# Kernel optimization log

Measured on AMD Instinct MI355X. Metric: run time of the kernel, lower is better.

The kernel has to match this reference:

```python
import jax, jax.numpy as jnp
import numpy as np

NTOKEN, NINP, NHID = 50257, 256, 256
B, T = 64, 2048
RES, FC1 = 10, NHID // 3
EPS = 1e-5

def lrelu(x, p=0.01):
    return jnp.maximum(x, x * p)

def setup_inputs() -> dict:
    key = jax.random.key(0)
    ks = jax.random.split(key, 12)
    s = 0.05
    inp = {
        "input": jax.random.randint(ks[0], (B, T), 0, NTOKEN),
        "hx": jnp.zeros((B, NHID), jnp.float32),
        "cx": jnp.zeros((B, NHID), jnp.float32),
        "seq_len": jax.random.randint(ks[1], (B,), 1, T + 1),  # lengths in [1, T]
        "emb_w": jax.random.uniform(ks[2], (NTOKEN, NINP), jnp.float32, -0.1, 0.1),
        "W_ih": jax.random.normal(ks[3], (4 * NHID, NINP), jnp.float32) * s,
        "W_hh": jax.random.normal(ks[4], (4 * NHID, NHID), jnp.float32) * s,
        "b_ih": jnp.zeros((4 * NHID,), jnp.float32),
        "b_hh": jnp.zeros((4 * NHID,), jnp.float32),
        "rfc1_w": jax.random.normal(ks[5], (RES, NHID), jnp.float32) * s,
        "rfc1_b": jnp.zeros((RES,), jnp.float32),
        "rbn_g": jnp.ones((RES,), jnp.float32),
        "rbn_b": jnp.zeros((RES,), jnp.float32),
        "rbn_rm": jnp.zeros((RES,), jnp.float32),
        "rbn_rv": jnp.ones((RES,), jnp.float32),
        "rfc2_w": jax.random.normal(ks[6], (NHID, RES), jnp.float32) * s,
        "rfc2_b": jnp.zeros((NHID,), jnp.float32),
        "fc1_w": jax.random.normal(ks[7], (FC1, NHID), jnp.float32) * s,
        "fc1_b": jnp.zeros((FC1,), jnp.float32),
        "bn1_g": jnp.ones((FC1,), jnp.float32),
        "bn1_b": jnp.zeros((FC1,), jnp.float32),
        "bn1_rm": jnp.zeros((FC1,), jnp.float32),
        "bn1_rv": jnp.ones((FC1,), jnp.float32),
        "fc2_w": jax.random.normal(ks[8], (2, FC1), jnp.float32) * s,
        "fc2_b": jnp.zeros((2,), jnp.float32),
    }
    return inp

def reference(input, hx, cx, seq_len, emb_w, W_ih, W_hh, b_ih, b_hh,
              rfc1_w, rfc1_b, rbn_g, rbn_b, rbn_rm, rbn_rv, rfc2_w, rfc2_b,
              fc1_w, fc1_b, bn1_g, bn1_b, bn1_rm, bn1_rv, fc2_w, fc2_b):
    # eval mode: dropout = identity, noise = 0, BatchNorm uses running stats
    emb = emb_w[input.T]  # [T, B, ninp]
    # precompute input-side gates once (batched matmul) -> [T, B, 4*nhid]
    x_gates = jnp.einsum('tbi,gi->tbg', emb, W_ih) + b_ih + b_hh

    def step(carry, xg):
        h, c = carry
        gates = xg + h @ W_hh.T
        i, f, g, o = jnp.split(gates, 4, axis=-1)
        c = jax.nn.sigmoid(f) * c + jax.nn.sigmoid(i) * jnp.tanh(g)
        h = jax.nn.sigmoid(o) * jnp.tanh(c)
        return (h, c), h

    (hx_f, cx_f), outs = jax.lax.scan(step, (hx, cx), x_gates)  # outs: [T, B, nhid]

    # ragged mean pooling over first seq_len[b] steps
    mask = (jnp.arange(T)[:, None] < seq_len[None, :]).astype(outs.dtype)  # [T, B]
    feature = jnp.einsum('tbh,tb->bh', outs, mask) / seq_len[:, None].astype(outs.dtype)

    # ResNet block (eval)
    res = jax.nn.relu(feature) @ rfc1_w.T + rfc1_b
    res = jax.nn.relu(res)
    res = (res - rbn_rm) * jax.lax.rsqrt(rbn_rv + EPS) * rbn_g + rbn_b
    feature = feature + res @ rfc2_w.T + rfc2_b

    # classifier head
    fc = feature @ fc1_w.T + fc1_b
    fc = (fc - bn1_rm) * jax.lax.rsqrt(bn1_rv + EPS) * bn1_g + bn1_b
    fc = lrelu(fc)
    logits = fc @ fc2_w.T + fc2_b
    logp = jax.nn.log_softmax(logits, axis=-1)
    return (logp, hx_f, cx_f)
```

## Files before the change

### kernel.cpp

```cpp
#include <hip/hip_runtime.h>
#include <cstdint>


#define NTOKEN 50257
#define NINP 256
#define NHID 256
#define BB 64
#define TT 2048
#define NRES 10
#define NFC1 85
#define EPSV 1e-5f

typedef _Float16 f16;
typedef _Float16 f16x2 __attribute__((ext_vector_type(2)));
typedef _Float16 f16x8 __attribute__((ext_vector_type(8)));
typedef float f32x4 __attribute__((ext_vector_type(4)));

static __device__ __forceinline__ float sigm(float x) { return 1.0f / (1.0f + __expf(-x)); }
static __device__ __forceinline__ float tanh_(float x) {
  float ax = fabsf(x);
  float e = __expf(-2.0f * ax);
  float t = (1.0f - e) / (1.0f + e);
  return x < 0.0f ? -t : t;
}

static __device__ __forceinline__ float fdot2(f16x2 a, f16x2 b, float c) {
#if __has_builtin(__builtin_amdgcn_fdot2)
  return __builtin_amdgcn_fdot2(a, b, c, false);
#else
  return c + (float)a[0] * (float)b[0] + (float)a[1] * (float)b[1];
#endif
}

__global__ void k0_convert(const float* __restrict__ emb_w, const float* __restrict__ W_ih,
                           const float* __restrict__ b_ih, const float* __restrict__ b_hh,
                           f16* __restrict__ emb16, f16* __restrict__ wih16,
                           float* __restrict__ bias) {
  int64_t i = (int64_t)blockIdx.x * blockDim.x + threadIdx.x;
  if (i < (int64_t)NTOKEN * NINP) emb16[i] = (f16)emb_w[i];
  if (i < 4 * NHID * NINP) wih16[i] = (f16)W_ih[i];
  if (i < 4 * NHID) bias[i] = b_ih[i] + b_hh[i];
}

__global__ __launch_bounds__(256) void k1_gemm(const f16* __restrict__ emb16,
                                               const f16* __restrict__ wih16,
                                               const float* __restrict__ bias,
                                               f16* __restrict__ xgtab) {
  __shared__ __align__(16) f16 a_lds[64][40];
  __shared__ __align__(16) f16 b_lds[256][40];
  const int mt = blockIdx.x;
  const int nt0 = blockIdx.y * 256;
  const int tid = threadIdx.x;
  const int lane = tid & 63;
  const int w = tid >> 6;
  const int quad = lane >> 4;
  const int l16 = lane & 15;

  f32x4 acc[16];
#pragma unroll
  for (int i = 0; i < 16; i++) acc[i] = (f32x4){0.f, 0.f, 0.f, 0.f};

  const int ar = tid >> 2;
  int av = mt * 64 + ar;
  if (av > NTOKEN - 1) av = NTOKEN - 1;
  const int ac = (tid & 3) * 8;

  for (int kb = 0; kb < 256; kb += 32) {
    *(uint4*)&a_lds[ar][ac] = *(const uint4*)&emb16[av * 256 + kb + ac];
    {
      const uint4* bs = (const uint4*)&wih16[(nt0 + tid) * 256 + kb];
      uint4* bd = (uint4*)&b_lds[tid][0];
      bd[0] = bs[0]; bd[1] = bs[1]; bd[2] = bs[2]; bd[3] = bs[3];
    }
    __syncthreads();
    f16x8 af = *(const f16x8*)&a_lds[w * 16 + l16][quad * 8];
#pragma unroll
    for (int nt = 0; nt < 16; nt++) {
      f16x8 bf = *(const f16x8*)&b_lds[nt * 16 + l16][quad * 8];
      acc[nt] = __builtin_amdgcn_mfma_f32_16x16x32_f16(af, bf, acc[nt], 0, 0, 0);
    }
    __syncthreads();
  }
#pragma unroll
  for (int nt = 0; nt < 16; nt++) {
#pragma unroll
    for (int rg = 0; rg < 4; rg++) {
      int v = mt * 64 + w * 16 + quad * 4 + rg;
      if (v < NTOKEN) {
        int n = nt0 + nt * 16 + l16;
        xgtab[v * 1024 + n] = (f16)(acc[nt][rg] + bias[n]);
      }
    }
  }
}

#define RK 100
#define LKW ((128 - RK) / 2)
__global__ __attribute__((amdgpu_flat_work_group_size(512, 512), amdgpu_waves_per_eu(2, 2)))
void k2_rnn(
    const int* __restrict__ input, const float* __restrict__ hx0,
    const float* __restrict__ cx0, const int* __restrict__ seq_len,
    const float* __restrict__ Whh, const f16* __restrict__ xgtab,
    float* __restrict__ feat, float* __restrict__ out_hx, float* __restrict__ out_cx) {
  __shared__ uint4 lw4[LKW * 512];
  __shared__ __align__(16) f16 hpak[2][NHID];

  const int b = blockIdx.x;
  const int tid = threadIdx.x;
  const int w = tid >> 6;
  const int lane = tid & 63;
  const int half = lane >> 5;
  const int p = w * 32 + (lane & 31);
  const int r0 = half ? (p + 256) : p;
  const int r1 = half ? (p + 768) : (p + 512);

  unsigned int w0[RK], w1[RK];
  unsigned int pa0 = 0, pd0 = 0;
#pragma unroll
  for (int m = 0; m < 128; m++) {
    float2 a = *(const float2*)&Whh[r0 * 256 + 2 * m];
    float2 d = *(const float2*)&Whh[r1 * 256 + 2 * m];
    f16x2 pa; pa[0] = (f16)a.x; pa[1] = (f16)a.y;
    f16x2 pd; pd[0] = (f16)d.x; pd[1] = (f16)d.y;
    unsigned int ua = __builtin_bit_cast(unsigned int, pa);
    unsigned int ud = __builtin_bit_cast(unsigned int, pd);
    if (m < RK) {
      w0[m] = ua; w1[m] = ud;
    } else if (((m - RK) & 1) == 0) {
      pa0 = ua; pd0 = ud;
    } else {
      lw4[((m - RK) >> 1) * 512 + tid] = make_uint4(pa0, pd0, ua, ud);
    }
  }

  float c = 0.0f, pool = 0.0f, hnew = 0.0f;
  if (tid < NHID) hpak[0][tid] = (f16)hx0[b * NHID + tid];
  if (!half) c = cx0[b * NHID + p];
  const int L = seq_len[b];
  __syncthreads();

  const int* tokp = input + b * TT;
  int tok_next = tokp[1];
  f16 xga, xgb;
  {
    int tok0 = tokp[0];
    xga = xgtab[tok0 * 1024 + r0];
    xgb = xgtab[tok0 * 1024 + r1];
  }

  for (int t = 0; t < TT; t++) {
    const int cur = t & 1;
    int tn = (t + 2 < TT) ? tokp[t + 2] : 0;
    f16 pfa = xgtab[tok_next * 1024 + r0];
    f16 pfb = xgtab[tok_next * 1024 + r1];

    float acc0 = (float)xga, acc1 = (float)xgb;
    const uint4* hp = (const uint4*)hpak[cur];
    uint4 hC = hp[0];
    uint4 hN = hp[1];
#pragma unroll
    for (int mb = 0; mb < 32; mb++) {
      uint4 h4 = hC;
      hC = hN;
      if (mb < 30) hN = hp[mb + 2];
      uint4 ww0, ww1;
      if (4 * mb >= RK) {
        ww0 = lw4[(2 * (mb - RK / 4)) * 512 + tid];
        ww1 = lw4[(2 * (mb - RK / 4) + 1) * 512 + tid];
      }
#pragma unroll
      for (int j = 0; j < 4; j++) {
        const int m = mb * 4 + j;
        unsigned int hu = (j == 0) ? h4.x : (j == 1) ? h4.y : (j == 2) ? h4.z : h4.w;
        f16x2 hh = __builtin_bit_cast(f16x2, hu);
        f16x2 wa, wb;
        if (m < RK) {
          wa = __builtin_bit_cast(f16x2, w0[m]);
          wb = __builtin_bit_cast(f16x2, w1[m]);
        } else {
          unsigned int uwa = (j == 0) ? ww0.x : (j == 1) ? ww0.z : (j == 2) ? ww1.x : ww1.z;
          unsigned int uwb = (j == 0) ? ww0.y : (j == 1) ? ww0.w : (j == 2) ? ww1.y : ww1.w;
          wa = __builtin_bit_cast(f16x2, uwa);
          wb = __builtin_bit_cast(f16x2, uwb);
        }
        acc0 = fdot2(wa, hh, acc0);
        acc1 = fdot2(wb, hh, acc1);
      }
    }

    float s0 = sigm(acc0);
    float oa = 0.0f;
    if (half) oa = sigm(acc1);
    float fs = __shfl_xor(half ? s0 : 0.0f, 32);
    float os = __shfl_xor(oa, 32);
    if (!half) {
      float gg = tanh_(acc1);
      c = fs * c + s0 * gg;
      hnew = os * tanh_(c);
      if (t < L) pool += hnew;
      hpak[cur ^ 1][p] = (f16)hnew;
    }
    __syncthreads();
    xga = pfa; xgb = pfb; tok_next = tn;
  }

  if (!half) {
    feat[b * NHID + p] = pool / (float)L;
    out_hx[b * NHID + p] = hnew;
    out_cx[b * NHID + p] = c;
  }
}

__global__ __launch_bounds__(256) void k3_head(const float* __restrict__ feat,
    const float* __restrict__ rfc1_w, const float* __restrict__ rfc1_b,
    const float* __restrict__ rbn_g, const float* __restrict__ rbn_b,
    const float* __restrict__ rbn_rm, const float* __restrict__ rbn_rv,
    const float* __restrict__ rfc2_w, const float* __restrict__ rfc2_b,
    const float* __restrict__ fc1_w, const float* __restrict__ fc1_b,
    const float* __restrict__ bn1_g, const float* __restrict__ bn1_b,
    const float* __restrict__ bn1_rm, const float* __restrict__ bn1_rv,
    const float* __restrict__ fc2_w, const float* __restrict__ fc2_b,
    float* __restrict__ logp) {
  __shared__ float f[256];
  __shared__ float f2[256];
  __shared__ float res[16];
  __shared__ float fcv[96];
  const int b = blockIdx.x, tid = threadIdx.x;
  const int wv = tid >> 6, lane = tid & 63;
  f[tid] = feat[b * 256 + tid];
  __syncthreads();
  for (int r = wv; r < NRES; r += 4) {
    float p = 0.f;
#pragma unroll
    for (int j0 = 0; j0 < 4; j0++) {
      int j = lane * 4 + j0;
      p += fmaxf(f[j], 0.f) * rfc1_w[r * 256 + j];
    }
    for (int off = 32; off > 0; off >>= 1) p += __shfl_down(p, off);
    if (lane == 0) {
      float x = p + rfc1_b[r];
      x = fmaxf(x, 0.f);
      x = (x - rbn_rm[r]) * rsqrtf(rbn_rv[r] + EPSV) * rbn_g[r] + rbn_b[r];
      res[r] = x;
    }
  }
  __syncthreads();
  {
    float s = rfc2_b[tid];
#pragma unroll
    for (int r = 0; r < NRES; r++) s += res[r] * rfc2_w[tid * NRES + r];
    f2[tid] = f[tid] + s;
  }
  __syncthreads();
  for (int o = wv; o < NFC1; o += 4) {
    float p = 0.f;
#pragma unroll
    for (int j0 = 0; j0 < 4; j0++) {
      int j = lane * 4 + j0;
      p += f2[j] * fc1_w[o * 256 + j];
    }
    for (int off = 32; off > 0; off >>= 1) p += __shfl_down(p, off);
    if (lane == 0) {
      float x = p + fc1_b[o];
      x = (x - bn1_rm[o]) * rsqrtf(bn1_rv[o] + EPSV) * bn1_g[o] + bn1_b[o];
      x = fmaxf(x, 0.01f * x);
      fcv[o] = x;
    }
  }
  __syncthreads();
  if (tid == 0) {
    float l0 = fc2_b[0], l1 = fc2_b[1];
    for (int o2 = 0; o2 < NFC1; o2++) {
      l0 += fcv[o2] * fc2_w[o2];
      l1 += fcv[o2] * fc2_w[NFC1 + o2];
    }
    float mx = fmaxf(l0, l1);
    float lse = mx + __logf(__expf(l0 - mx) + __expf(l1 - mx));
    logp[b * 2 + 0] = l0 - lse;
    logp[b * 2 + 1] = l1 - lse;
  }
}

extern "C" void kernel_launch(void* const* d_in, const int* in_sizes, int n_in,
                              void* d_out, int out_size, void* d_ws, size_t ws_size,
                              hipStream_t stream) {
  const int*   input  = (const int*)  d_in[0];
  const float* hx     = (const float*)d_in[1];
  const float* cx     = (const float*)d_in[2];
  const int*   seqlen = (const int*)  d_in[3];
  const float* emb_w  = (const float*)d_in[4];
  const float* W_ih   = (const float*)d_in[5];
  const float* W_hh   = (const float*)d_in[6];
  const float* b_ih   = (const float*)d_in[7];
  const float* b_hh   = (const float*)d_in[8];
  const float* rfc1_w = (const float*)d_in[9];
  const float* rfc1_b = (const float*)d_in[10];
  const float* rbn_g  = (const float*)d_in[11];
  const float* rbn_b  = (const float*)d_in[12];
  const float* rbn_rm = (const float*)d_in[13];
  const float* rbn_rv = (const float*)d_in[14];
  const float* rfc2_w = (const float*)d_in[15];
  const float* rfc2_b = (const float*)d_in[16];
  const float* fc1_w  = (const float*)d_in[17];
  const float* fc1_b  = (const float*)d_in[18];
  const float* bn1_g  = (const float*)d_in[19];
  const float* bn1_b  = (const float*)d_in[20];
  const float* bn1_rm = (const float*)d_in[21];
  const float* bn1_rv = (const float*)d_in[22];
  const float* fc2_w  = (const float*)d_in[23];
  const float* fc2_b  = (const float*)d_in[24];

  char* ws = (char*)d_ws;
  f16*   emb16 = (f16*)(ws);
  f16*   wih16 = (f16*)(ws + 25731584);
  float* bias  = (float*)(ws + 26255872);
  f16*   xgtab = (f16*)(ws + 26259968);
  float* feat  = (float*)(ws + 129186304);

  float* out = (float*)d_out;

  k0_convert<<<dim3(NTOKEN), 256, 0, stream>>>(emb_w, W_ih, b_ih, b_hh, emb16, wih16, bias);
  k1_gemm<<<dim3((NTOKEN + 63) / 64, 4), 256, 0, stream>>>(emb16, wih16, bias, xgtab);
  k2_rnn<<<dim3(BB), 512, 0, stream>>>(input, hx, cx, seqlen, W_hh, xgtab, feat,
                                       out + 128, out + 128 + BB * NHID);
  k3_head<<<dim3(BB), 256, 0, stream>>>(feat, rfc1_w, rfc1_b, rbn_g, rbn_b, rbn_rm, rbn_rv,
                                        rfc2_w, rfc2_b, fc1_w, fc1_b, bn1_g, bn1_b, bn1_rm,
                                        bn1_rv, fc2_w, fc2_b, out);
}
```

Before: 3.936 ms.

## Split LSTM recurrence to one gate row per thread with interleaved gate layout

Each recurrent block now launches 1024 threads, each owning a single W_hh gate row. Previously 512 threads each handled two rows. The GEMM epilogue writes the precomputed input-gate table interleaved so the four gates of a hidden unit sit in adjacent lanes, and adjacent-lane shuffles combine them. This halves the serial dot-product chain per thread on every timestep, which is the latency-critical path of the recurrence. The costs are more threads synchronising each step, tighter register budgets (90 register-resident weight pairs under a 1024-thread bound), and a changed xgtab layout that every consumer must agree on.

```diff
diff --git a/kernel.cpp b/kernel.cpp
--- a/kernel.cpp
+++ b/kernel.cpp
@@ -10,6 +10,9 @@
 #define NRES 10
 #define NFC1 85
 #define EPSV 1e-5f
+
+#define RK 90
+#define LSLOT ((128 - RK) / 2)
 
 typedef _Float16 f16;
 typedef _Float16 f16x2 __attribute__((ext_vector_type(2)));
@@ -88,126 +91,108 @@
       int v = mt * 64 + w * 16 + quad * 4 + rg;
       if (v < NTOKEN) {
         int n = nt0 + nt * 16 + l16;
-        xgtab[v * 1024 + n] = (f16)(acc[nt][rg] + bias[n]);
+        xgtab[v * 1024 + nt * 64 + l16 * 4 + blockIdx.y] = (f16)(acc[nt][rg] + bias[n]);
       }
     }
   }
 }
 
-#define RK 100
-#define LKW ((128 - RK) / 2)
-__global__ __attribute__((amdgpu_flat_work_group_size(512, 512), amdgpu_waves_per_eu(2, 2)))
-void k2_rnn(
-    const int* __restrict__ input, const float* __restrict__ hx0,
-    const float* __restrict__ cx0, const int* __restrict__ seq_len,
-    const float* __restrict__ Whh, const f16* __restrict__ xgtab,
-    float* __restrict__ feat, float* __restrict__ out_hx, float* __restrict__ out_cx) {
-  __shared__ uint4 lw4[LKW * 512];
+__global__ __launch_bounds__(1024, 4)
+void k2_rnn(const int* __restrict__ input, const float* __restrict__ hx0,
+            const float* __restrict__ cx0, const int* __restrict__ seq_len,
+            const float* __restrict__ Whh, const f16* __restrict__ xgtab,
+            float* __restrict__ feat, float* __restrict__ out_hx,
+            float* __restrict__ out_cx) {
+  __shared__ uint2 lw2[LSLOT * 1024];
   __shared__ __align__(16) f16 hpak[2][NHID];
 
   const int b = blockIdx.x;
   const int tid = threadIdx.x;
-  const int w = tid >> 6;
-  const int lane = tid & 63;
-  const int half = lane >> 5;
-  const int p = w * 32 + (lane & 31);
-  const int r0 = half ? (p + 256) : p;
-  const int r1 = half ? (p + 768) : (p + 512);
-
-  unsigned int w0[RK], w1[RK];
-  unsigned int pa0 = 0, pd0 = 0;
-#pragma unroll
-  for (int m = 0; m < 128; m++) {
-    float2 a = *(const float2*)&Whh[r0 * 256 + 2 * m];
-    float2 d = *(const float2*)&Whh[r1 * 256 + 2 * m];
-    f16x2 pa; pa[0] = (f16)a.x; pa[1] = (f16)a.y;
-    f16x2 pd; pd[0] = (f16)d.x; pd[1] = (f16)d.y;
-    unsigned int ua = __builtin_bit_cast(unsigned int, pa);
-    unsigned int ud = __builtin_bit_cast(unsigned int, pd);
-    if (m < RK) {
-      w0[m] = ua; w1[m] = ud;
-    } else if (((m - RK) & 1) == 0) {
-      pa0 = ua; pd0 = ud;
-    } else {
-      lw4[((m - RK) >> 1) * 512 + tid] = make_uint4(pa0, pd0, ua, ud);
-    }
-  }
-
-  float c = 0.0f, pool = 0.0f, hnew = 0.0f;
-  if (tid < NHID) hpak[0][tid] = (f16)hx0[b * NHID + tid];
-  if (!half) c = cx0[b * NHID + p];
+  const int g = tid & 3;
+  const int u = tid >> 2;
+  const int row = g * 256 + u;
+
+  unsigned int wr[RK];
+  unsigned int pend = 0;
+#pragma unroll
+  for (int m = 0; m < 128; ++m) {
+    float2 a = *(const float2*)&Whh[row * 256 + 2 * m];
+    f16x2 p; p[0] = (f16)a.x; p[1] = (f16)a.y;
+    unsigned int ua = __builtin_bit_cast(unsigned int, p);
+    if (m < RK) wr[m] = ua;
+    else if (((m - RK) & 1) == 0) pend = ua;
+    else lw2[((m - RK) >> 1) * 1024 + tid] = make_uint2(pend, ua);
+  }
+
+  float c = 0.f, pool = 0.f, hlast = 0.f;
+  if (g == 0) {
+    hpak[0][u] = (f16)hx0[b * NHID + u];
+    c = cx0[b * NHID + u];
+  }
   const int L = seq_len[b];
-  __syncthreads();
-
   const int* tokp = input + b * TT;
-  int tok_next = tokp[1];
-  f16 xga, xgb;
-  {
-    int tok0 = tokp[0];
-    xga = xgtab[tok0 * 1024 + r0];
-    xgb = xgtab[tok0 * 1024 + r1];
-  }
-
-  for (int t = 0; t < TT; t++) {
+  int toknx = tokp[1];
+  f16 xgc = xgtab[(int64_t)tokp[0] * 1024 + tid];
+  __syncthreads();
+
+#pragma unroll 1
+  for (int t = 0; t < TT; ++t) {
     const int cur = t & 1;
-    int tn = (t + 2 < TT) ? tokp[t + 2] : 0;
-    f16 pfa = xgtab[tok_next * 1024 + r0];
-    f16 pfb = xgtab[tok_next * 1024 + r1];
-
-    float acc0 = (float)xga, acc1 = (float)xgb;
+
+    f16 xgn = xgtab[(int64_t)toknx * 1024 + tid];
+    const int tok2 = tokp[(t + 2 < TT) ? (t + 2) : (TT - 1)];
+
+    float acc = (float)xgc;
     const uint4* hp = (const uint4*)hpak[cur];
     uint4 hC = hp[0];
     uint4 hN = hp[1];
-#pragma unroll
-    for (int mb = 0; mb < 32; mb++) {
+    uint2 lwv = {0u, 0u};
+#pragma unroll
+    for (int mb = 0; mb < 32; ++mb) {
       uint4 h4 = hC;
       hC = hN;
       if (mb < 30) hN = hp[mb + 2];
-      uint4 ww0, ww1;
-      if (4 * mb >= RK) {
-        ww0 = lw4[(2 * (mb - RK / 4)) * 512 + tid];
-        ww1 = lw4[(2 * (mb - RK / 4) + 1) * 512 + tid];
-      }
-#pragma unroll
-      for (int j = 0; j < 4; j++) {
+#pragma unroll
+      for (int j = 0; j < 4; ++j) {
         const int m = mb * 4 + j;
         unsigned int hu = (j == 0) ? h4.x : (j == 1) ? h4.y : (j == 2) ? h4.z : h4.w;
         f16x2 hh = __builtin_bit_cast(f16x2, hu);
-        f16x2 wa, wb;
+        unsigned int wu;
         if (m < RK) {
-          wa = __builtin_bit_cast(f16x2, w0[m]);
-          wb = __builtin_bit_cast(f16x2, w1[m]);
+          wu = wr[m];
         } else {
-          unsigned int uwa = (j == 0) ? ww0.x : (j == 1) ? ww0.z : (j == 2) ? ww1.x : ww1.z;
-          unsigned int uwb = (j == 0) ? ww0.y : (j == 1) ? ww0.w : (j == 2) ? ww1.y : ww1.w;
-          wa = __builtin_bit_cast(f16x2, uwa);
-          wb = __builtin_bit_cast(f16x2, uwb);
+          const int q = m - RK;
+          if ((q & 1) == 0) {
+            lwv = lw2[(q >> 1) * 1024 + tid];
+            wu = lwv.x;
+          } else {
+            wu = lwv.y;
+          }
         }
-        acc0 = fdot2(wa, hh, acc0);
-        acc1 = fdot2(wb, hh, acc1);
+        acc = fdot2(__builtin_bit_cast(f16x2, wu), hh, acc);
       }
     }
 
-    float s0 = sigm(acc0);
-    float oa = 0.0f;
-    if (half) oa = sigm(acc1);
-    float fs = __shfl_xor(half ? s0 : 0.0f, 32);
-    float os = __shfl_xor(oa, 32);
-    if (!half) {
-      float gg = tanh_(acc1);
-      c = fs * c + s0 * gg;
-      hnew = os * tanh_(c);
-      if (t < L) pool += hnew;
-      hpak[cur ^ 1][p] = (f16)hnew;
-    }
+    float sv = sigm(acc);
+    float act = (g == 2) ? tanh_(acc) : sv;
+    float fch = __shfl_down(act, 1);
+    float gch = __shfl_down(act, 2);
+    float och = __shfl_down(act, 3);
+    if (g == 0) {
+      c = fch * c + act * gch;
+      hlast = och * tanh_(c);
+      if (t < L) pool += hlast;
+      hpak[cur ^ 1][u] = (f16)hlast;
+    }
+    xgc = xgn;
+    toknx = tok2;
     __syncthreads();
-    xga = pfa; xgb = pfb; tok_next = tn;
-  }
-
-  if (!half) {
-    feat[b * NHID + p] = pool / (float)L;
-    out_hx[b * NHID + p] = hnew;
-    out_cx[b * NHID + p] = c;
+  }
+
+  if (g == 0) {
+    feat[b * NHID + u] = pool / (float)L;
+    out_hx[b * NHID + u] = hlast;
+    out_cx[b * NHID + u] = c;
   }
 }
 
@@ -321,8 +306,8 @@
 
   k0_convert<<<dim3(NTOKEN), 256, 0, stream>>>(emb_w, W_ih, b_ih, b_hh, emb16, wih16, bias);
   k1_gemm<<<dim3((NTOKEN + 63) / 64, 4), 256, 0, stream>>>(emb16, wih16, bias, xgtab);
-  k2_rnn<<<dim3(BB), 512, 0, stream>>>(input, hx, cx, seqlen, W_hh, xgtab, feat,
-                                       out + 128, out + 128 + BB * NHID);
+  k2_rnn<<<dim3(BB), 1024, 0, stream>>>(input, hx, cx, seqlen, W_hh, xgtab, feat,
+                                        out + 128, out + 128 + BB * NHID);
   k3_head<<<dim3(BB), 256, 0, stream>>>(feat, rfc1_w, rfc1_b, rbn_g, rbn_b, rbn_rm, rbn_rv,
                                         rfc2_w, rfc2_b, fc1_w, fc1_b, bn1_g, bn1_b, bn1_rm,
                                         bn1_rv, fc2_w, fc2_b, out);
```

Result: slower. 4.687 ms (+19.1%).
